# Optimization experiments

Measured on AMD Instinct MI355X. Metric: run time of the kernel, lower is better.

Reference implementation:

```python
import jax, jax.numpy as jnp
import numpy as np

D = 1024
NP = 128
BS = 2
GEO = 64
TOPK = 18

def _lin(x, w, b):
    return x @ w + b

def _mlp3(x, w1, b1, w2, b2, w3, b3):
    h = jax.nn.relu(_lin(x, w1, b1))
    h = jax.nn.relu(_lin(h, w2, b2))
    return _lin(h, w3, b3)


def setup_inputs() -> dict:
    key = jax.random.key(0)
    ks = jax.random.split(key, 24)
    feats = jax.random.normal(ks[0], (BS, NP, D), jnp.float32)
    subject = jax.random.normal(ks[1], (BS, D), jnp.float32)
    obj = jax.random.normal(ks[2], (BS, D), jnp.float32)
    # plausible boxes: xmin,ymin in [0,500), w,h in [1,101)
    xy = jax.random.uniform(ks[3], (BS, NP, 2), jnp.float32) * 500.0
    wh = jax.random.uniform(ks[4], (BS, NP, 2), jnp.float32) * 100.0 + 1.0
    prop = jnp.concatenate([xy, xy + wh], axis=-1)
    s = 0.02
    p = {}
    for i, k in zip((1, 2, 3), ks[5:8]):
        p[f"gp_w{i}"] = jax.random.normal(k, (GEO, GEO), jnp.float32) * s
        p[f"gp_b{i}"] = jnp.zeros((GEO,), jnp.float32)
    # pass_messgae: Linear(2112,1024), Linear(1024,1024), Linear(1024,1024)
    dims = [(2 * D + GEO, D), (D, D), (D, D)]
    for i, (k, (di, do)) in enumerate(zip(ks[8:11], dims), 1):
        p[f"pm_w{i}"] = jax.random.normal(k, (di, do), jnp.float32) * s
        p[f"pm_b{i}"] = jnp.zeros((do,), jnp.float32)
    # aggregate: Linear(2048,1024), Linear(1024,1024), Linear(1024,1024)
    dims = [(2 * D, D), (D, D), (D, D)]
    for i, (k, (di, do)) in enumerate(zip(ks[11:14], dims), 1):
        p[f"ag_w{i}"] = jax.random.normal(k, (di, do), jnp.float32) * s
        p[f"ag_b{i}"] = jnp.zeros((do,), jnp.float32)
    p["cs_w"] = jax.random.normal(ks[14], (2 * D, 1), jnp.float32) * s
    p["cs_b"] = jnp.zeros((1,), jnp.float32)
    p["cso_w"] = jax.random.normal(ks[15], (2 * D, 1), jnp.float32) * s
    p["cso_b"] = jnp.zeros((1,), jnp.float32)
    return dict(feats=feats, subject=subject, obj=obj, prop=prop, **p)


def _geo_embedding(prop):
    # extract_multi_position_matrix_nd with S == O == prop
    xmin, ymin, xmax, ymax = jnp.split(prop, 4, axis=-1)  # [bs,np,1]
    w = xmax - xmin + 1.0
    h = ymax - ymin + 1.0
    cx = 0.5 * (xmin + xmax)
    cy = 0.5 * (ymin + ymax)
    # [bs, np_S, np_O]
    dx = (cx - jnp.swapaxes(cx, 1, 2)) / jnp.swapaxes(w, 1, 2)
    dy = (cy - jnp.swapaxes(cy, 1, 2)) / jnp.swapaxes(h, 1, 2)
    dw = w / jnp.swapaxes(w, 1, 2)
    dh = h / jnp.swapaxes(h, 1, 2)
    pos = jnp.stack([dx, dy, dw, dh], axis=3)  # [bs,np,np,4]
    pos = jnp.log(jnp.maximum(jnp.abs(pos), 1e-3))
    # extract_pairwise_multi_position_embedding_nd, feat_dim=64, wave_length=1000
    feat_range = jnp.arange(GEO // 8, dtype=pos.dtype)
    dim_mat = jnp.power(jnp.asarray(1000.0, pos.dtype), (8.0 / GEO) * feat_range)  # [8]
    div = (100.0 * pos)[..., None] / dim_mat  # [bs,np,np,4,8]
    emb = jnp.concatenate([jnp.sin(div), jnp.cos(div)], axis=-1)  # [bs,np,np,4,16]
    return emb.reshape(*emb.shape[:3], GEO)  # [bs,np,np,64]


def reference(feats, subject, obj, prop,
              gp_w1, gp_b1, gp_w2, gp_b2, gp_w3, gp_b3,
              pm_w1, pm_b1, pm_w2, pm_b2, pm_w3, pm_b3,
              ag_w1, ag_b1, ag_w2, ag_b2, ag_w3, ag_b3,
              cs_w, cs_b, cso_w, cso_b):
    bs, num_prop, d = feats.shape
    geo = _geo_embedding(prop)                        # [bs,np,np,64]
    geo = _mlp3(geo, gp_w1, gp_b1, gp_w2, gp_b2, gp_w3, gp_b3)
    # x_1[b,i,j]=feats[b,j] ; x_2[b,i,j]=feats[b,i]  (torch unsqueeze/repeat)
    shp = (bs, num_prop, num_prop, d)
    x1 = jnp.broadcast_to(feats[:, None, :, :], shp)
    x2 = jnp.broadcast_to(feats[:, :, None, :], shp)
    pair = jnp.concatenate([x1, x2, geo], axis=-1)    # [bs,np,np,2112]
    fet = _mlp3(pair, pm_w1, pm_b1, pm_w2, pm_b2, pm_w3, pm_b3)  # [bs,np,np,1024]
    # topk over dim=2 then sum/8
    top, _ = jax.lax.top_k(jnp.swapaxes(fet, 2, 3), TOPK)  # [bs,np,1024,18]
    fet = top.sum(axis=-1) / 8.0                      # [bs,np,1024]
    x = _mlp3(jnp.concatenate([feats, fet], axis=-1),
              ag_w1, ag_b1, ag_w2, ag_b2, ag_w3, ag_b3)  # [bs,np,1024]
    sub = jnp.broadcast_to(subject[:, None, :], (bs, num_prop, d))
    ob = jnp.broadcast_to(obj[:, None, :], (bs, num_prop, d))
    x_subj = jax.nn.sigmoid(_lin(jnp.concatenate([x, sub], -1), cs_w, cs_b))[..., 0]
    x_obj = jax.nn.sigmoid(_lin(jnp.concatenate([x, ob], -1), cso_w, cso_b))[..., 0]
    return jnp.stack([x_subj, x_obj], axis=-1)        # [bs,np,2]
```

## Files before the change

kernel.cpp:

```cpp
#include <hip/hip_runtime.h>
#include <hip/hip_bf16.h>
#include <math.h>

#define D 1024
#define NP 128
#define BS 2
#define GEO 64
#define TOPKN 18
#define NPAIR (BS*NP*NP)

__device__ __forceinline__ float relu_(float x){ return fmaxf(x, 0.f); }
__device__ __forceinline__ unsigned short f2b(float x){
    __hip_bfloat16 h = __float2bfloat16(x);
    return *(unsigned short*)&h;
}
__device__ __forceinline__ float b2f(unsigned short u){
    return __uint_as_float((unsigned)u << 16);
}

typedef short bf16x8 __attribute__((ext_vector_type(8)));
typedef float f32x4  __attribute__((ext_vector_type(4)));

__device__ __forceinline__ void glds16(const unsigned short* g, unsigned short* l){
    __builtin_amdgcn_global_load_lds(
        (const __attribute__((address_space(1))) void*)g,
        (__attribute__((address_space(3))) void*)l,
        16, 0, 0);
}

#define GSTR 72
__global__ __launch_bounds__(256) void k_geo2(
    const float* __restrict__ prop,
    const float* __restrict__ gw1, const float* __restrict__ gb1,
    const float* __restrict__ gw2, const float* __restrict__ gb2,
    const float* __restrict__ gw3, const float* __restrict__ gb3,
    unsigned short* __restrict__ geoPc, int pofs)
{
    __shared__ unsigned short WT[3][GEO*GSTR];
    __shared__ float gb[3][GEO];
    __shared__ unsigned short buf[4][GEO*GSTR];
    int t = threadIdx.x, l = t & 63, w = t >> 6;

    for (int idx = t; idx < GEO*GEO; idx += 256) {
        int k = idx >> 6, n = idx & 63;
        WT[0][n*GSTR + k] = f2b(gw1[idx]);
        WT[1][n*GSTR + k] = f2b(gw2[idx]);
        WT[2][n*GSTR + k] = f2b(gw3[idx]);
    }
    if (t < GEO) { gb[0][t]=gb1[t]; gb[1][t]=gb2[t]; gb[2][t]=gb3[t]; }

    int plocal = blockIdx.x*256 + w*64;
    int pair0  = pofs + plocal;
    int c = l;
    int p = c >> 4, s = c & 15, f = s & 7;
    float dm = expf((float)f * (6.907755278982137f/8.0f));
    bool is_cos = (s & 8) != 0;
    float scale = 100.f / dm;

    int b  = pair0 >> 14;
    int ij = pair0 & 16383;
    int i  = ij >> 7;
    int j0 = ij & 127;
    float4 pi = *(const float4*)(prop + (size_t)(b*NP + i)*4);
    float wi  = pi.z-pi.x+1.f, hi_ = pi.w-pi.y+1.f;
    unsigned short* mybuf = buf[w];
    for (int r = 0; r < 64; ++r) {
        float4 pj = *(const float4*)(prop + (size_t)(b*NP + j0 + r)*4);
        float wj  = pj.z-pj.x+1.f, hj  = pj.w-pj.y+1.f;
        float pos;
        if      (p == 0) pos = (0.5f*(pi.x+pi.z) - 0.5f*(pj.x+pj.z)) / wj;
        else if (p == 1) pos = (0.5f*(pi.y+pi.w) - 0.5f*(pj.y+pj.w)) / hj;
        else if (p == 2) pos = wi / wj;
        else             pos = hi_ / hj;
        pos = logf(fmaxf(fabsf(pos), 1e-3f));
        float dv = pos * scale;
        mybuf[r*GSTR + c] = f2b(is_cos ? cosf(dv) : sinf(dv));
    }
    __syncthreads();

    int lr = l & 15, lq = l >> 4;
    #pragma unroll
    for (int layer = 0; layer < 3; ++layer) {
        const unsigned short* WTl = WT[layer];
        f32x4 acc[4][4];
        #pragma unroll
        for (int mi = 0; mi < 4; ++mi)
            #pragma unroll
            for (int ni = 0; ni < 4; ++ni)
                #pragma unroll
                for (int r = 0; r < 4; ++r) acc[mi][ni][r] = 0.f;
        #pragma unroll
        for (int kc = 0; kc < 2; ++kc) {
            bf16x8 af[4], bf[4];
            #pragma unroll
            for (int mi = 0; mi < 4; ++mi)
                af[mi] = *(const bf16x8*)(mybuf + (mi*16+lr)*GSTR + kc*32 + lq*8);
            #pragma unroll
            for (int ni = 0; ni < 4; ++ni)
                bf[ni] = *(const bf16x8*)(WTl + (ni*16+lr)*GSTR + kc*32 + lq*8);
            #pragma unroll
            for (int mi = 0; mi < 4; ++mi)
                #pragma unroll
                for (int ni = 0; ni < 4; ++ni)
                    acc[mi][ni] = __builtin_amdgcn_mfma_f32_16x16x32_bf16(af[mi], bf[ni], acc[mi][ni], 0, 0, 0);
        }
        __syncthreads();
        #pragma unroll
        for (int mi = 0; mi < 4; ++mi) {
            #pragma unroll
            for (int ni = 0; ni < 4; ++ni) {
                int col = ni*16 + lr;
                float bv = gb[layer][col];
                #pragma unroll
                for (int r = 0; r < 4; ++r) {
                    int row = mi*16 + lq*4 + r;
                    float v = acc[mi][ni][r] + bv;
                    if (layer < 2) {
                        mybuf[row*GSTR + col] = f2b(relu_(v));
                    } else {
                        geoPc[(size_t)(plocal + row)*GEO + col] = f2b(v);
                    }
                }
            }
        }
        __syncthreads();
    }
}

struct WT8 {
    const float* src[8];
    unsigned short* dst[8];
    int kt[8];
    int pre[9];
};
__global__ __launch_bounds__(256) void k_wTall(WT8 d)
{
    __shared__ float tile[64][65];
    int bid = blockIdx.x;
    int e = 0;
    while (e < 7 && bid >= d.pre[e+1]) ++e;
    int local = bid - d.pre[e];
    int bx = local & 15;
    int by = local >> 4;
    int K = d.kt[e] * 64;
    const float* W = d.src[e];
    unsigned short* WT = d.dst[e];
    int t = threadIdx.x;
    int tc = t & 63, tr = t >> 6;
    #pragma unroll
    for (int r = tr; r < 64; r += 4)
        tile[r][tc] = W[(size_t)(by*64 + r)*1024 + bx*64 + tc];
    __syncthreads();
    #pragma unroll
    for (int r = tr; r < 64; r += 4)
        WT[(size_t)(bx*64 + r)*K + by*64 + tc] = f2b(tile[tc][r]);
}

template<bool A_F32>
__global__ __launch_bounds__(256) void k_skmm(
    const void* __restrict__ A1v, const void* __restrict__ A2v,
    int K1, int K2,
    const unsigned short* __restrict__ BT0,
    const unsigned short* __restrict__ BT1,
    float* __restrict__ Cp,
    int KZ, int Kc, int N)
{
    __shared__ unsigned short As[16*32];
    __shared__ unsigned short Bs[128*32];
    int t = threadIdx.x;
    int m0 = blockIdx.x * 16;
    int n0 = blockIdx.y * 128;
    int bz = blockIdx.z;
    int kz = bz % KZ;
    int mat = bz / KZ;
    const unsigned short* BT = mat ? BT1 : BT0;
    int K = K1 + K2;
    int M = gridDim.x * 16;
    int w = t >> 6, l = t & 63;
    int lr = l & 15, lq = l >> 4;
    int arow = t >> 3, ak = (t & 7) * 4;
    int arow2 = t >> 2, ak2 = (t & 3) * 8;
    int brow = t >> 1, bk = (t & 1) * 16;
    f32x4 acc0 = {0.f,0.f,0.f,0.f}, acc1 = {0.f,0.f,0.f,0.f};
    for (int i = 0; i < Kc; i += 32) {
        int kg0 = kz*Kc + i;
        __syncthreads();
        if (A_F32) {
            if (t < 128) {
                int kg = kg0 + ak;
                const float* src = (kg < K1)
                    ? (const float*)A1v + (size_t)(m0+arow)*K1 + kg
                    : (const float*)A2v + (size_t)(m0+arow)*K2 + (kg - K1);
                float4 a4 = *(const float4*)src;
                ushort4 u;
                u.x=f2b(a4.x); u.y=f2b(a4.y); u.z=f2b(a4.z); u.w=f2b(a4.w);
                *(ushort4*)(As + arow*32 + ak) = u;
            }
        } else {
            if (t < 64) {
                const unsigned short* src = (const unsigned short*)A1v + (size_t)(m0+arow2)*K1 + kg0 + ak2;
                *(bf16x8*)(As + arow2*32 + ak2) = *(const bf16x8*)src;
            }
        }
        const unsigned short* srcb = BT + (size_t)(n0+brow)*K + kg0 + bk;
        *(bf16x8*)(Bs + brow*32 + bk)     = *(const bf16x8*)srcb;
        *(bf16x8*)(Bs + brow*32 + bk + 8) = *(const bf16x8*)(srcb + 8);
        __syncthreads();
        bf16x8 af = *(const bf16x8*)(As + lr*32 + lq*8);
        bf16x8 b0 = *(const bf16x8*)(Bs + (w*32      + lr)*32 + lq*8);
        bf16x8 b1 = *(const bf16x8*)(Bs + (w*32 + 16 + lr)*32 + lq*8);
        acc0 = __builtin_amdgcn_mfma_f32_16x16x32_bf16(af, b0, acc0, 0, 0, 0);
        acc1 = __builtin_amdgcn_mfma_f32_16x16x32_bf16(af, b1, acc1, 0, 0, 0);
    }
    float* Co = Cp + (size_t)bz*M*N;
    #pragma unroll
    for (int r = 0; r < 4; ++r) {
        int gr = m0 + lq*4 + r;
        Co[(size_t)gr*N + n0 + w*32      + lr] = acc0[r];
        Co[(size_t)gr*N + n0 + w*32 + 16 + lr] = acc1[r];
    }
}

template<bool RELU, bool OUT_BF16>
__global__ __launch_bounds__(256) void k_red(
    const float* __restrict__ Cp, int KZ,
    const float* __restrict__ bias,
    void* __restrict__ out0, void* __restrict__ out1,
    int MN, int N)
{
    int z = blockIdx.z;
    const float* C = Cp + (size_t)z*KZ*MN;
    void* out = z ? out1 : out0;
    int idx = (blockIdx.x*256 + threadIdx.x) * 4;
    f32x4 s = {0.f,0.f,0.f,0.f};
    for (int k = 0; k < KZ; ++k)
        s += *(const f32x4*)(C + (size_t)k*MN + idx);
    if (bias) s += *(const f32x4*)(bias + (idx & (N-1)));
    if (RELU) { s[0]=relu_(s[0]); s[1]=relu_(s[1]); s[2]=relu_(s[2]); s[3]=relu_(s[3]); }
    if (OUT_BF16) {
        ushort4 u; u.x=f2b(s[0]); u.y=f2b(s[1]); u.z=f2b(s[2]); u.w=f2b(s[3]);
        *(ushort4*)((unsigned short*)out + idx) = u;
    } else {
        float4 o; o.x=s[0]; o.y=s[1]; o.z=s[2]; o.w=s[3];
        *(float4*)((float*)out + idx) = o;
    }
}


#define STG(g, lb) { glds16((g) + ssrc0, (lb) + sdst0); glds16((g) + ssrc1, (lb) + sdst1); }

#define MM8_PHASE(Q, LAH, LBH, STAGE_STMT, VM)                                  \
  {                                                                             \
    if ((Q) == 0 || (Q) == 2) {                                                 \
      const char* ah = (const char*)(LAH) + ((Q) == 2 ? 16384 : 0);             \
      _Pragma("unroll")                                                         \
      for (int mi = 0; mi < 4; ++mi) {                                          \
        af[mi][0] = *(const bf16x8*)(ah + aoff[mi][0]);                         \
        af[mi][1] = *(const bf16x8*)(ah + aoff[mi][1]);                         \
      }                                                                         \
    }                                                                           \
    if ((Q) != 2) {                                                             \
      const char* bh = (const char*)(LBH) + ((Q) == 1 ? 16384 : 0);             \
      _Pragma("unroll")                                                         \
      for (int ni = 0; ni < 2; ++ni) {                                          \
        bfr[ni][0] = *(const bf16x8*)(bh + boff[ni][0]);                        \
        bfr[ni][1] = *(const bf16x8*)(bh + boff[ni][1]);                        \
      }                                                                         \
    }                                                                           \
    STAGE_STMT;                                                                 \
    asm volatile("s_waitcnt vmcnt(" #VM ")" ::: "memory");                      \
    __builtin_amdgcn_s_barrier();                                               \
    asm volatile("" ::: "memory");                                              \
    __builtin_amdgcn_s_setprio(1);                                              \
    _Pragma("unroll")                                                           \
    for (int mi = 0; mi < 4; ++mi)                                              \
      _Pragma("unroll")                                                         \
      for (int ni = 0; ni < 2; ++ni) {                                          \
        const int am = ((Q) >= 2 ? 4 : 0) + mi;                                 \
        const int an = (((Q) == 1 || (Q) == 2) ? 2 : 0) + ni;                   \
        acc[am][an] = __builtin_amdgcn_mfma_f32_16x16x32_bf16(af[mi][0], bfr[ni][0], acc[am][an], 0, 0, 0); \
        acc[am][an] = __builtin_amdgcn_mfma_f32_16x16x32_bf16(af[mi][1], bfr[ni][1], acc[am][an], 0, 0, 0); \
      }                                                                         \
    __builtin_amdgcn_s_setprio(0);                                              \
  }

template<bool RELU>
__global__ __launch_bounds__(512, 2) void k_mgemm8(
    const unsigned short* __restrict__ A,
    const unsigned short* __restrict__ BT,
    const float* __restrict__ bias,
    unsigned short* __restrict__ C, int M, int N, int K)
{
    __shared__ __align__(16) unsigned short LA[2][2][128*64];
    __shared__ __align__(16) unsigned short LB[2][2][128*64];
    int t = threadIdx.x;

    int nwg = gridDim.x * gridDim.y;
    int bid = blockIdx.y * gridDim.x + blockIdx.x;
    int wgid = (nwg & 7) ? bid : ((bid & 7) * (nwg >> 3) + (bid >> 3));
    int ntm = M >> 8;
    int tm = wgid % ntm, tn = wgid / ntm;
    int m0 = tm << 8, n0 = tn << 8;

    int w = t >> 6, l = t & 63;
    int wm = w & 1, wn = w >> 1;
    int lr = l & 15, lq = l >> 4;

    const unsigned short* Abase = A  + (size_t)m0 * K;
    const unsigned short* Bbase = BT + (size_t)n0 * K;
    int NT = K >> 6;

    size_t ssrc0, ssrc1; int sdst0, sdst1;
    {
        int o0 = t * 16;
        int s0 = o0 ^ (((o0 >> 7) & 7) << 4);
        ssrc0 = (size_t)(s0 >> 7)*K + ((s0 & 127) >> 1);
        sdst0 = o0 >> 1;
        int o1 = (512 + t) * 16;
        int s1 = o1 ^ (((o1 >> 7) & 7) << 4);
        ssrc1 = (size_t)(s1 >> 7)*K + ((s1 & 127) >> 1);
        sdst1 = o1 >> 1;
    }

    int aoff[4][2], boff[2][2];
    #pragma unroll
    for (int mi = 0; mi < 4; ++mi)
        #pragma unroll
        for (int kq = 0; kq < 2; ++kq) {
            int lo = (wm*64 + mi*16 + lr)*128 + kq*64 + lq*16;
            aoff[mi][kq] = lo ^ (((lo >> 7) & 7) << 4);
        }
    #pragma unroll
    for (int ni = 0; ni < 2; ++ni)
        #pragma unroll
        for (int kq = 0; kq < 2; ++kq) {
            int lo = (wn*32 + ni*16 + lr)*128 + kq*64 + lq*16;
            boff[ni][kq] = lo ^ (((lo >> 7) & 7) << 4);
        }

    f32x4 acc[8][4];
    #pragma unroll
    for (int i = 0; i < 8; ++i)
        #pragma unroll
        for (int j = 0; j < 4; ++j)
            #pragma unroll
            for (int r = 0; r < 4; ++r) acc[i][j][r] = 0.f;

    bf16x8 af[4][2], bfr[2][2];

    STG(Abase,                  &LA[0][0][0]);
    STG(Bbase,                  &LB[0][0][0]);
    STG(Bbase + (size_t)128*K,  &LB[0][1][0]);
    STG(Abase + (size_t)128*K,  &LA[0][1][0]);
    asm volatile("s_waitcnt vmcnt(4)" ::: "memory");
    __builtin_amdgcn_s_barrier();
    asm volatile("" ::: "memory");

    for (int kt = 0; kt < NT - 1; ++kt) {
        const unsigned short* la = &LA[kt & 1][0][0];
        const unsigned short* lb = &LB[kt & 1][0][0];
        unsigned short* nla = &LA[(kt + 1) & 1][0][0];
        unsigned short* nlb = &LB[(kt + 1) & 1][0][0];
        const unsigned short* An = Abase + (size_t)((kt + 1) << 6);
        const unsigned short* Bn = Bbase + (size_t)((kt + 1) << 6);
        MM8_PHASE(0, la, lb, STG(An, nla), 4);
        MM8_PHASE(1, la, lb, STG(Bn, nlb), 4);
        MM8_PHASE(2, la, lb, STG(Bn + (size_t)128*K, nlb + 8192), 4);
        MM8_PHASE(3, la, lb, STG(An + (size_t)128*K, nla + 8192), 4);
    }
    {
        const unsigned short* la = &LA[(NT - 1) & 1][0][0];
        const unsigned short* lb = &LB[(NT - 1) & 1][0][0];
        MM8_PHASE(0, la, lb, (void)0, 2);
        MM8_PHASE(1, la, lb, (void)0, 0);
        MM8_PHASE(2, la, lb, (void)0, 0);
        MM8_PHASE(3, la, lb, (void)0, 0);
    }

    #pragma unroll
    for (int mi = 0; mi < 8; ++mi) {
        int grow = m0 + ((mi & 4) ? 128 : 0) + wm*64 + (mi & 3)*16 + lq*4;
        #pragma unroll
        for (int ni = 0; ni < 4; ++ni) {
            int gcol = n0 + ((ni & 2) ? 128 : 0) + wn*32 + (ni & 1)*16 + lr;
            float bv = bias[gcol];
            #pragma unroll
            for (int r = 0; r < 4; ++r) {
                float v = acc[mi][ni][r] + bv;
                if (RELU) v = relu_(v);
                C[(size_t)(grow + r)*N + gcol] = f2b(v);
            }
        }
    }
}

__global__ __launch_bounds__(256) void k_h1m(
    const unsigned short* __restrict__ A,
    const unsigned short* __restrict__ BT,
    const float* __restrict__ b1,
    const unsigned short* __restrict__ U, const unsigned short* __restrict__ V,
    unsigned short* __restrict__ h1c, int pofs)
{
    __shared__ unsigned short As[2*128*32];
    __shared__ unsigned short Bs[2*128*32];
    const int K = GEO;
    int t  = threadIdx.x;
    int m0 = blockIdx.x * 128;
    int n0 = blockIdx.y * 128;
    int w  = t >> 6, l = t & 63;
    int wm = w & 1, wn = w >> 1;
    int lr = l & 15;
    int lq = l >> 4;

    int s0 = w*2, s1 = w*2 + 1;
    int srow = l >> 2;
    int sko  = (l & 3) * 8;
    int rowA0 = s0*16 + srow, rowA1 = s1*16 + srow;

    f32x4 acc[4][4];
    #pragma unroll
    for (int mi = 0; mi < 4; ++mi)
        #pragma unroll
        for (int ni = 0; ni < 4; ++ni)
            #pragma unroll
            for (int r = 0; r < 4; ++r) acc[mi][ni][r] = 0.f;

    #pragma unroll
    for (int q = 0; q < 2; ++q) {
        int kg = q*32 + sko;
        glds16(A  + (size_t)(m0 + rowA0)*K + kg, As + q*4096 + s0*512 + l*8);
        glds16(A  + (size_t)(m0 + rowA1)*K + kg, As + q*4096 + s1*512 + l*8);
        glds16(BT + (size_t)(n0 + rowA0)*K + kg, Bs + q*4096 + s0*512 + l*8);
        glds16(BT + (size_t)(n0 + rowA1)*K + kg, Bs + q*4096 + s1*512 + l*8);
    }
    __syncthreads();
    #pragma unroll
    for (int q = 0; q < 2; ++q) {
        bf16x8 af[4], bf[4];
        #pragma unroll
        for (int mi = 0; mi < 4; ++mi)
            af[mi] = *(const bf16x8*)(As + q*4096 + (wm*64 + mi*16 + lr)*32 + lq*8);
        #pragma unroll
        for (int ni = 0; ni < 4; ++ni)
            bf[ni] = *(const bf16x8*)(Bs + q*4096 + (wn*64 + ni*16 + lr)*32 + lq*8);
        #pragma unroll
        for (int mi = 0; mi < 4; ++mi)
            #pragma unroll
            for (int ni = 0; ni < 4; ++ni)
                acc[mi][ni] = __builtin_amdgcn_mfma_f32_16x16x32_bf16(af[mi], bf[ni], acc[mi][ni], 0, 0, 0);
    }

    int p0 = pofs + m0;
    int bi = p0 >> 7;
    int b  = bi >> 7;
    const unsigned short* Ubase = U + (size_t)b*NP*D;
    const unsigned short* Vrow  = V + (size_t)bi*D;
    #pragma unroll
    for (int ni = 0; ni < 4; ++ni) {
        int gc = n0 + wn*64 + ni*16 + lr;
        float add = b2f(Vrow[gc]) + b1[gc];
        #pragma unroll
        for (int mi = 0; mi < 4; ++mi) {
            int row = wm*64 + mi*16 + lq*4;
            #pragma unroll
            for (int r = 0; r < 4; ++r) {
                float u = b2f(Ubase[(size_t)(row + r)*D + gc]);
                float val = acc[mi][ni][r] + u + add;
                h1c[(size_t)(m0 + row + r)*D + gc] = f2b(relu_(val));
            }
        }
    }
}

#define TK_PAD 19
__global__ __launch_bounds__(256) void k_topk2(
    const unsigned short* __restrict__ fcb,
    float* __restrict__ red_out)
{
    __shared__ float L1[256][TK_PAD];
    __shared__ float L2[128][TK_PAD];
    int t = threadIdx.x;
    int bl = blockIdx.x;
    int cbase = blockIdx.y * 64;
    int cl = t & 63;
    int q = t >> 6;
    const unsigned short* base = fcb + (size_t)(bl*NP + q*32)*D + cbase + cl;
    float sm[TOPKN];
    #pragma unroll
    for (int x = 0; x < TOPKN; ++x) sm[x] = -INFINITY;
    for (int j = 0; j < 32; ++j) {
        float v = b2f(base[(size_t)j*D]);
        #pragma unroll
        for (int x = 0; x < TOPKN; ++x) {
            float mx = fmaxf(sm[x], v);
            v = fminf(sm[x], v);
            sm[x] = mx;
        }
    }
    #pragma unroll
    for (int x = 0; x < TOPKN; ++x) L1[t][x] = sm[x];
    __syncthreads();
    if (t < 128) {
        int h = t >> 6, cc = t & 63;
        const float* la = L1[(2*h)*64 + cc];
        const float* lb = L1[(2*h+1)*64 + cc];
        float* dst = L2[h*64 + cc];
        int ia = 0, ib = 0;
        float av = la[0], bv = lb[0];
        #pragma unroll
        for (int x = 0; x < TOPKN; ++x) {
            bool ta = (av >= bv);
            dst[x] = ta ? av : bv;
            if (ta) { ++ia; av = (ia < TOPKN) ? la[ia] : -INFINITY; }
            else    { ++ib; bv = (ib < TOPKN) ? lb[ib] : -INFINITY; }
        }
    }
    __syncthreads();
    if (t < 64) {
        const float* la = L2[t];
        const float* lb = L2[64 + t];
        int ia = 0, ib = 0;
        float av = la[0], bv = lb[0];
        float s = 0.f;
        #pragma unroll
        for (int x = 0; x < TOPKN; ++x) {
            bool ta = (av >= bv);
            s += ta ? av : bv;
            if (ta) { ++ia; av = (ia < TOPKN) ? la[ia] : -INFINITY; }
            else    { ++ib; bv = (ib < TOPKN) ? lb[ib] : -INFINITY; }
        }
        red_out[(size_t)bl*D + cbase + t] = s * 0.125f;
    }
}

__global__ __launch_bounds__(256) void k_final(const float* __restrict__ x,
    const float* __restrict__ subject, const float* __restrict__ obj,
    const float* __restrict__ cs_w, const float* __restrict__ cs_b,
    const float* __restrict__ cso_w, const float* __restrict__ cso_b,
    float* __restrict__ out)
{
    int bi = blockIdx.x;
    int b  = bi >> 7;
    const float* xr = x + (size_t)bi*D;
    const float* sb = subject + (size_t)b*D;
    const float* ob = obj + (size_t)b*D;
    int tid = threadIdx.x;
    float a0 = 0.f, a1 = 0.f;
    for (int k = tid; k < D; k += 256) {
        float xv = xr[k];
        a0 = fmaf(xv, cs_w[k], a0);
        a0 = fmaf(sb[k], cs_w[D+k], a0);
        a1 = fmaf(xv, cso_w[k], a1);
        a1 = fmaf(ob[k], cso_w[D+k], a1);
    }
    __shared__ float r0[256], r1[256];
    r0[tid] = a0; r1[tid] = a1;
    __syncthreads();
    for (int s2 = 128; s2 > 0; s2 >>= 1) {
        if (tid < s2) { r0[tid] += r0[tid+s2]; r1[tid] += r1[tid+s2]; }
        __syncthreads();
    }
    if (tid == 0) {
        out[bi*2+0] = 1.f/(1.f + expf(-(r0[0] + cs_b[0])));
        out[bi*2+1] = 1.f/(1.f + expf(-(r1[0] + cso_b[0])));
    }
}

extern "C" void kernel_launch(void* const* d_in, const int* in_sizes, int n_in,
                              void* d_out, int out_size, void* d_ws, size_t ws_size,
                              hipStream_t stream)
{
    const float* feats   = (const float*)d_in[0];
    const float* subject = (const float*)d_in[1];
    const float* obj     = (const float*)d_in[2];
    const float* prop    = (const float*)d_in[3];
    const float* gp_w1 = (const float*)d_in[4];  const float* gp_b1 = (const float*)d_in[5];
    const float* gp_w2 = (const float*)d_in[6];  const float* gp_b2 = (const float*)d_in[7];
    const float* gp_w3 = (const float*)d_in[8];  const float* gp_b3 = (const float*)d_in[9];
    const float* pm_w1 = (const float*)d_in[10]; const float* pm_b1 = (const float*)d_in[11];
    const float* pm_w2 = (const float*)d_in[12]; const float* pm_b2 = (const float*)d_in[13];
    const float* pm_w3 = (const float*)d_in[14]; const float* pm_b3 = (const float*)d_in[15];
    const float* ag_w1 = (const float*)d_in[16]; const float* ag_b1 = (const float*)d_in[17];
    const float* ag_w2 = (const float*)d_in[18]; const float* ag_b2 = (const float*)d_in[19];
    const float* ag_w3 = (const float*)d_in[20]; const float* ag_b3 = (const float*)d_in[21];
    const float* cs_w  = (const float*)d_in[22]; const float* cs_b  = (const float*)d_in[23];
    const float* cso_w = (const float*)d_in[24]; const float* cso_b = (const float*)d_in[25];
    float* out = (float*)d_out;

    const int M = BS*NP;
    const int MN = M*D;

    char* wsb = (char*)d_ws;
    size_t off = 0;
    auto alloc = [&](size_t bytes) { char* p = wsb + off; off += (bytes + 255) & ~255ull; return p; };
    unsigned short* Ub = (unsigned short*)alloc((size_t)MN*2);
    unsigned short* Vb = (unsigned short*)alloc((size_t)MN*2);
    float* red = (float*)alloc((size_t)MN*4);
    float* xf  = (float*)alloc((size_t)MN*4);
    unsigned short* xh1b = (unsigned short*)alloc((size_t)MN*2);
    unsigned short* xh2b = (unsigned short*)alloc((size_t)MN*2);
    unsigned short* w1aT = (unsigned short*)alloc((size_t)D*D*2);
    unsigned short* w1bT = (unsigned short*)alloc((size_t)D*D*2);
    unsigned short* w1cT = (unsigned short*)alloc((size_t)D*GEO*2);
    unsigned short* w2T  = (unsigned short*)alloc((size_t)D*D*2);
    unsigned short* w3T  = (unsigned short*)alloc((size_t)D*D*2);
    unsigned short* agw1T= (unsigned short*)alloc((size_t)2*D*D*2);
    unsigned short* agw2T= (unsigned short*)alloc((size_t)D*D*2);
    unsigned short* agw3T= (unsigned short*)alloc((size_t)D*D*2);
    size_t persist = off;

    size_t cp_bytes = (size_t)8*MN*4;
    size_t chunk_unit = (size_t)NP*(GEO*2 + D*2 + D*2 + D*2);
    int CH = M;
    while (CH > 2) {
        size_t region = (size_t)CH*chunk_unit;
        if (region < cp_bytes) region = cp_bytes;
        if (persist + region + 4096 <= ws_size) break;
        CH >>= 1;
    }
    float*          Cp    = (float*)(wsb + persist);
    unsigned short* geoPc = (unsigned short*)(wsb + persist);
    unsigned short* h1c   = geoPc + (size_t)CH*NP*GEO;
    unsigned short* h2c   = h1c   + (size_t)CH*NP*D;
    unsigned short* fcb   = h2c   + (size_t)CH*NP*D;

    WT8 d;
    d.src[0]=pm_w1;                d.dst[0]=w1aT;  d.kt[0]=16;
    d.src[1]=pm_w1+(size_t)D*D;    d.dst[1]=w1bT;  d.kt[1]=16;
    d.src[2]=pm_w1+(size_t)2*D*D;  d.dst[2]=w1cT;  d.kt[2]=1;
    d.src[3]=pm_w2;                d.dst[3]=w2T;   d.kt[3]=16;
    d.src[4]=pm_w3;                d.dst[4]=w3T;   d.kt[4]=16;
    d.src[5]=ag_w1;                d.dst[5]=agw1T; d.kt[5]=32;
    d.src[6]=ag_w2;                d.dst[6]=agw2T; d.kt[6]=16;
    d.src[7]=ag_w3;                d.dst[7]=agw3T; d.kt[7]=16;
    d.pre[0]=0;
    for (int e = 0; e < 8; ++e) d.pre[e+1] = d.pre[e] + d.kt[e]*16;
    k_wTall<<<d.pre[8], 256, 0, stream>>>(d);

    k_skmm<true><<<dim3(M/16, D/128, 8), 256, 0, stream>>>(
        feats, nullptr, D, 0, w1aT, w1bT, Cp, 4, 256, D);
    k_red<false,true><<<dim3(MN/1024, 1, 2), 256, 0, stream>>>(
        Cp, 4, nullptr, Ub, Vb, MN, D);

    int nchunks = M/CH;
    for (int cchunk = 0; cchunk < nchunks; ++cchunk) {
        int bi0  = cchunk * CH;
        int pofs = bi0 * NP;
        k_geo2<<<CH*NP/256, 256, 0, stream>>>(prop, gp_w1, gp_b1, gp_w2, gp_b2, gp_w3, gp_b3, geoPc, pofs);
        dim3 gBig(CH*NP/128, D/128);
        k_h1m<<<gBig, 256, 0, stream>>>(geoPc, w1cT, pm_b1, Ub, Vb, h1c, pofs);
        dim3 g8(CH*NP/256, D/256);
        k_mgemm8<true ><<<g8, 512, 0, stream>>>(h1c, w2T, pm_b2, h2c, CH*NP, D, D);
        k_mgemm8<false><<<g8, 512, 0, stream>>>(h2c, w3T, pm_b3, fcb, CH*NP, D, D);
        k_topk2<<<dim3(CH, D/64), 256, 0, stream>>>(fcb, red + (size_t)bi0*D);
    }

    k_skmm<true><<<dim3(M/16, D/128, 8), 256, 0, stream>>>(
        feats, red, D, D, agw1T, nullptr, Cp, 8, 256, D);
    k_red<true,true><<<dim3(MN/1024, 1, 1), 256, 0, stream>>>(
        Cp, 8, ag_b1, xh1b, nullptr, MN, D);
    k_skmm<false><<<dim3(M/16, D/128, 4), 256, 0, stream>>>(
        xh1b, nullptr, D, 0, agw2T, nullptr, Cp, 4, 256, D);
    k_red<true,true><<<dim3(MN/1024, 1, 1), 256, 0, stream>>>(
        Cp, 4, ag_b2, xh2b, nullptr, MN, D);
    k_skmm<false><<<dim3(M/16, D/128, 4), 256, 0, stream>>>(
        xh2b, nullptr, D, 0, agw3T, nullptr, Cp, 4, 256, D);
    k_red<false,false><<<dim3(MN/1024, 1, 1), 256, 0, stream>>>(
        Cp, 4, ag_b3, xf, nullptr, MN, D);

    k_final<<<M, 256, 0, stream>>>(xf, subject, obj, cs_w, cs_b, cso_w, cso_b, out);
}
```

Before: 461.5 us.

## Replace split-K skinny GEMMs plus reduction kernels with fused full-K GEMM epilogue

The small M=256 GEMMs (feature projections and the aggregate MLP) drop split-K partial buffers and their separate reduction kernels. Each block now loops over the full K, staging two 32-wide K slices per iteration in shared memory, and applies bias, ReLU and the bf16 conversion directly in the epilogue. This removes four reduction launches and the fp32 partial-sum traffic, and lets the chunk buffer ignore the Cp size floor. The cost is far fewer blocks (16x8 or 16x8x2), so parallelism drops and each block runs a long serial K loop.

```diff
diff --git a/kernel.cpp b/kernel.cpp
--- a/kernel.cpp
+++ b/kernel.cpp
@@ -156,93 +156,81 @@
         WT[(size_t)(bx*64 + r)*K + by*64 + tc] = f2b(tile[tc][r]);
 }
 
-template<bool A_F32>
-__global__ __launch_bounds__(256) void k_skmm(
+template<bool A_F32, bool RELU, bool OUT_BF16>
+__global__ __launch_bounds__(256) void k_skd(
     const void* __restrict__ A1v, const void* __restrict__ A2v,
     int K1, int K2,
     const unsigned short* __restrict__ BT0,
     const unsigned short* __restrict__ BT1,
-    float* __restrict__ Cp,
-    int KZ, int Kc, int N)
-{
-    __shared__ unsigned short As[16*32];
-    __shared__ unsigned short Bs[128*32];
+    const float* __restrict__ bias,
+    void* __restrict__ out0, void* __restrict__ out1, int N)
+{
+    __shared__ unsigned short As[2][16*32];
+    __shared__ unsigned short Bs[2][128*32];
     int t = threadIdx.x;
     int m0 = blockIdx.x * 16;
     int n0 = blockIdx.y * 128;
-    int bz = blockIdx.z;
-    int kz = bz % KZ;
-    int mat = bz / KZ;
+    int mat = blockIdx.z;
     const unsigned short* BT = mat ? BT1 : BT0;
+    void* outp = mat ? out1 : out0;
     int K = K1 + K2;
-    int M = gridDim.x * 16;
     int w = t >> 6, l = t & 63;
     int lr = l & 15, lq = l >> 4;
     int arow = t >> 3, ak = (t & 7) * 4;
     int arow2 = t >> 2, ak2 = (t & 3) * 8;
     int brow = t >> 1, bk = (t & 1) * 16;
     f32x4 acc0 = {0.f,0.f,0.f,0.f}, acc1 = {0.f,0.f,0.f,0.f};
-    for (int i = 0; i < Kc; i += 32) {
-        int kg0 = kz*Kc + i;
+    for (int i = 0; i < K; i += 64) {
         __syncthreads();
-        if (A_F32) {
-            if (t < 128) {
-                int kg = kg0 + ak;
-                const float* src = (kg < K1)
-                    ? (const float*)A1v + (size_t)(m0+arow)*K1 + kg
-                    : (const float*)A2v + (size_t)(m0+arow)*K2 + (kg - K1);
-                float4 a4 = *(const float4*)src;
-                ushort4 u;
-                u.x=f2b(a4.x); u.y=f2b(a4.y); u.z=f2b(a4.z); u.w=f2b(a4.w);
-                *(ushort4*)(As + arow*32 + ak) = u;
+        #pragma unroll
+        for (int h = 0; h < 2; ++h) {
+            int kg0 = i + h*32;
+            if (A_F32) {
+                if (t < 128) {
+                    int kg = kg0 + ak;
+                    const float* src = (kg < K1)
+                        ? (const float*)A1v + (size_t)(m0+arow)*K1 + kg
+                        : (const float*)A2v + (size_t)(m0+arow)*K2 + (kg - K1);
+                    float4 a4 = *(const float4*)src;
+                    ushort4 u;
+                    u.x=f2b(a4.x); u.y=f2b(a4.y); u.z=f2b(a4.z); u.w=f2b(a4.w);
+                    *(ushort4*)(As[h] + arow*32 + ak) = u;
+                }
+            } else {
+                if (t < 64) {
+                    const unsigned short* src = (const unsigned short*)A1v + (size_t)(m0+arow2)*K1 + kg0 + ak2;
+                    *(bf16x8*)(As[h] + arow2*32 + ak2) = *(const bf16x8*)src;
+                }
             }
+            const unsigned short* srcb = BT + (size_t)(n0+brow)*K + kg0 + bk;
+            *(bf16x8*)(Bs[h] + brow*32 + bk)     = *(const bf16x8*)srcb;
+            *(bf16x8*)(Bs[h] + brow*32 + bk + 8) = *(const bf16x8*)(srcb + 8);
+        }
+        __syncthreads();
+        #pragma unroll
+        for (int h = 0; h < 2; ++h) {
+            bf16x8 af = *(const bf16x8*)(As[h] + lr*32 + lq*8);
+            bf16x8 b0 = *(const bf16x8*)(Bs[h] + (w*32      + lr)*32 + lq*8);
+            bf16x8 b1 = *(const bf16x8*)(Bs[h] + (w*32 + 16 + lr)*32 + lq*8);
+            acc0 = __builtin_amdgcn_mfma_f32_16x16x32_bf16(af, b0, acc0, 0, 0, 0);
+            acc1 = __builtin_amdgcn_mfma_f32_16x16x32_bf16(af, b1, acc1, 0, 0, 0);
+        }
+    }
+    #pragma unroll
+    for (int r = 0; r < 4; ++r) {
+        int gr  = m0 + lq*4 + r;
+        int gc0 = n0 + w*32 + lr;
+        int gc1 = gc0 + 16;
+        float v0 = acc0[r] + (bias ? bias[gc0] : 0.f);
+        float v1 = acc1[r] + (bias ? bias[gc1] : 0.f);
+        if (RELU) { v0 = relu_(v0); v1 = relu_(v1); }
+        if (OUT_BF16) {
+            ((unsigned short*)outp)[(size_t)gr*N + gc0] = f2b(v0);
+            ((unsigned short*)outp)[(size_t)gr*N + gc1] = f2b(v1);
         } else {
-            if (t < 64) {
-                const unsigned short* src = (const unsigned short*)A1v + (size_t)(m0+arow2)*K1 + kg0 + ak2;
-                *(bf16x8*)(As + arow2*32 + ak2) = *(const bf16x8*)src;
-            }
-        }
-        const unsigned short* srcb = BT + (size_t)(n0+brow)*K + kg0 + bk;
-        *(bf16x8*)(Bs + brow*32 + bk)     = *(const bf16x8*)srcb;
-        *(bf16x8*)(Bs + brow*32 + bk + 8) = *(const bf16x8*)(srcb + 8);
-        __syncthreads();
-        bf16x8 af = *(const bf16x8*)(As + lr*32 + lq*8);
-        bf16x8 b0 = *(const bf16x8*)(Bs + (w*32      + lr)*32 + lq*8);
-        bf16x8 b1 = *(const bf16x8*)(Bs + (w*32 + 16 + lr)*32 + lq*8);
-        acc0 = __builtin_amdgcn_mfma_f32_16x16x32_bf16(af, b0, acc0, 0, 0, 0);
-        acc1 = __builtin_amdgcn_mfma_f32_16x16x32_bf16(af, b1, acc1, 0, 0, 0);
-    }
-    float* Co = Cp + (size_t)bz*M*N;
-    #pragma unroll
-    for (int r = 0; r < 4; ++r) {
-        int gr = m0 + lq*4 + r;
-        Co[(size_t)gr*N + n0 + w*32      + lr] = acc0[r];
-        Co[(size_t)gr*N + n0 + w*32 + 16 + lr] = acc1[r];
-    }
-}
-
-template<bool RELU, bool OUT_BF16>
-__global__ __launch_bounds__(256) void k_red(
-    const float* __restrict__ Cp, int KZ,
-    const float* __restrict__ bias,
-    void* __restrict__ out0, void* __restrict__ out1,
-    int MN, int N)
-{
-    int z = blockIdx.z;
-    const float* C = Cp + (size_t)z*KZ*MN;
-    void* out = z ? out1 : out0;
-    int idx = (blockIdx.x*256 + threadIdx.x) * 4;
-    f32x4 s = {0.f,0.f,0.f,0.f};
-    for (int k = 0; k < KZ; ++k)
-        s += *(const f32x4*)(C + (size_t)k*MN + idx);
-    if (bias) s += *(const f32x4*)(bias + (idx & (N-1)));
-    if (RELU) { s[0]=relu_(s[0]); s[1]=relu_(s[1]); s[2]=relu_(s[2]); s[3]=relu_(s[3]); }
-    if (OUT_BF16) {
-        ushort4 u; u.x=f2b(s[0]); u.y=f2b(s[1]); u.z=f2b(s[2]); u.w=f2b(s[3]);
-        *(ushort4*)((unsigned short*)out + idx) = u;
-    } else {
-        float4 o; o.x=s[0]; o.y=s[1]; o.z=s[2]; o.w=s[3];
-        *(float4*)((float*)out + idx) = o;
+            ((float*)outp)[(size_t)gr*N + gc0] = v0;
+            ((float*)outp)[(size_t)gr*N + gc1] = v1;
+        }
     }
 }
 
@@ -609,16 +597,13 @@
     unsigned short* agw3T= (unsigned short*)alloc((size_t)D*D*2);
     size_t persist = off;
 
-    size_t cp_bytes = (size_t)8*MN*4;
     size_t chunk_unit = (size_t)NP*(GEO*2 + D*2 + D*2 + D*2);
     int CH = M;
     while (CH > 2) {
         size_t region = (size_t)CH*chunk_unit;
-        if (region < cp_bytes) region = cp_bytes;
         if (persist + region + 4096 <= ws_size) break;
         CH >>= 1;
     }
-    float*          Cp    = (float*)(wsb + persist);
     unsigned short* geoPc = (unsigned short*)(wsb + persist);
     unsigned short* h1c   = geoPc + (size_t)CH*NP*GEO;
     unsigned short* h2c   = h1c   + (size_t)CH*NP*D;
@@ -637,10 +622,8 @@
     for (int e = 0; e < 8; ++e) d.pre[e+1] = d.pre[e] + d.kt[e]*16;
     k_wTall<<<d.pre[8], 256, 0, stream>>>(d);
 
-    k_skmm<true><<<dim3(M/16, D/128, 8), 256, 0, stream>>>(
-        feats, nullptr, D, 0, w1aT, w1bT, Cp, 4, 256, D);
-    k_red<false,true><<<dim3(MN/1024, 1, 2), 256, 0, stream>>>(
-        Cp, 4, nullptr, Ub, Vb, MN, D);
+    k_skd<true,false,true><<<dim3(M/16, D/128, 2), 256, 0, stream>>>(
+        feats, nullptr, D, 0, w1aT, w1bT, nullptr, Ub, Vb, D);
 
     int nchunks = M/CH;
     for (int cchunk = 0; cchunk < nchunks; ++cchunk) {
@@ -655,18 +638,12 @@
         k_topk2<<<dim3(CH, D/64), 256, 0, stream>>>(fcb, red + (size_t)bi0*D);
     }
 
-    k_skmm<true><<<dim3(M/16, D/128, 8), 256, 0, stream>>>(
-        feats, red, D, D, agw1T, nullptr, Cp, 8, 256, D);
-    k_red<true,true><<<dim3(MN/1024, 1, 1), 256, 0, stream>>>(
-        Cp, 8, ag_b1, xh1b, nullptr, MN, D);
-    k_skmm<false><<<dim3(M/16, D/128, 4), 256, 0, stream>>>(
-        xh1b, nullptr, D, 0, agw2T, nullptr, Cp, 4, 256, D);
-    k_red<true,true><<<dim3(MN/1024, 1, 1), 256, 0, stream>>>(
-        Cp, 4, ag_b2, xh2b, nullptr, MN, D);
-    k_skmm<false><<<dim3(M/16, D/128, 4), 256, 0, stream>>>(
-        xh2b, nullptr, D, 0, agw3T, nullptr, Cp, 4, 256, D);
-    k_red<false,false><<<dim3(MN/1024, 1, 1), 256, 0, stream>>>(
-        Cp, 4, ag_b3, xf, nullptr, MN, D);
+    k_skd<true,true,true><<<dim3(M/16, D/128, 1), 256, 0, stream>>>(
+        feats, red, D, D, agw1T, nullptr, ag_b1, xh1b, nullptr, D);
+    k_skd<false,true,true><<<dim3(M/16, D/128, 1), 256, 0, stream>>>(
+        xh1b, nullptr, D, 0, agw2T, nullptr, ag_b2, xh2b, nullptr, D);
+    k_skd<false,false,false><<<dim3(M/16, D/128, 1), 256, 0, stream>>>(
+        xh2b, nullptr, D, 0, agw3T, nullptr, ag_b3, xf, nullptr, D);
 
     k_final<<<M, 256, 0, stream>>>(xf, subject, obj, cs_w, cs_b, cso_w, cso_b, out);
 }
```

Measured after the change: 512.0 us. +10.9%, slower.

## Fuse top-k reduction into final pass-message GEMM epilogue

Applied to the files above, without the earlier changes.

The third pass-message GEMM no longer writes its bf16 output to global memory for a separate top-k kernel. Instead, each 256x256 tile transposes its accumulators through shared memory, and 256 threads each run an insertion top-18 over the 128 rows of one column, writing the scaled sum directly. This removes a large global write and read plus one kernel launch, and the smaller per-chunk workspace may allow bigger chunks. In exchange, shared memory grows to about 135KB, which may limit occupancy, the top-k phase runs on only half the threads, and top-k now sees fp32 values rather than bf16-rounded ones.

```diff
diff --git a/kernel.cpp b/kernel.cpp
--- a/kernel.cpp
+++ b/kernel.cpp
@@ -284,15 +284,16 @@
     __builtin_amdgcn_s_setprio(0);                                              \
   }
 
-template<bool RELU>
+template<bool RELU, bool TOPK>
 __global__ __launch_bounds__(512, 2) void k_mgemm8(
     const unsigned short* __restrict__ A,
     const unsigned short* __restrict__ BT,
     const float* __restrict__ bias,
-    unsigned short* __restrict__ C, int M, int N, int K)
-{
-    __shared__ __align__(16) unsigned short LA[2][2][128*64];
-    __shared__ __align__(16) unsigned short LB[2][2][128*64];
+    void* __restrict__ Cv, int M, int N, int K)
+{
+    __shared__ __align__(16) char SMEM[256*132*4];
+    unsigned short* LAp = (unsigned short*)SMEM;
+    unsigned short* LBp = LAp + 32768;
     int t = threadIdx.x;
 
     int nwg = gridDim.x * gridDim.y;
@@ -348,19 +349,19 @@
 
     bf16x8 af[4][2], bfr[2][2];
 
-    STG(Abase,                  &LA[0][0][0]);
-    STG(Bbase,                  &LB[0][0][0]);
-    STG(Bbase + (size_t)128*K,  &LB[0][1][0]);
-    STG(Abase + (size_t)128*K,  &LA[0][1][0]);
+    STG(Abase,                  LAp);
+    STG(Bbase,                  LBp);
+    STG(Bbase + (size_t)128*K,  LBp + 8192);
+    STG(Abase + (size_t)128*K,  LAp + 8192);
     asm volatile("s_waitcnt vmcnt(4)" ::: "memory");
     __builtin_amdgcn_s_barrier();
     asm volatile("" ::: "memory");
 
     for (int kt = 0; kt < NT - 1; ++kt) {
-        const unsigned short* la = &LA[kt & 1][0][0];
-        const unsigned short* lb = &LB[kt & 1][0][0];
-        unsigned short* nla = &LA[(kt + 1) & 1][0][0];
-        unsigned short* nlb = &LB[(kt + 1) & 1][0][0];
+        const unsigned short* la = LAp + (kt & 1)*16384;
+        const unsigned short* lb = LBp + (kt & 1)*16384;
+        unsigned short* nla = LAp + ((kt + 1) & 1)*16384;
+        unsigned short* nlb = LBp + ((kt + 1) & 1)*16384;
         const unsigned short* An = Abase + (size_t)((kt + 1) << 6);
         const unsigned short* Bn = Bbase + (size_t)((kt + 1) << 6);
         MM8_PHASE(0, la, lb, STG(An, nla), 4);
@@ -369,26 +370,71 @@
         MM8_PHASE(3, la, lb, STG(An + (size_t)128*K, nla + 8192), 4);
     }
     {
-        const unsigned short* la = &LA[(NT - 1) & 1][0][0];
-        const unsigned short* lb = &LB[(NT - 1) & 1][0][0];
+        const unsigned short* la = LAp + ((NT - 1) & 1)*16384;
+        const unsigned short* lb = LBp + ((NT - 1) & 1)*16384;
         MM8_PHASE(0, la, lb, (void)0, 2);
         MM8_PHASE(1, la, lb, (void)0, 0);
         MM8_PHASE(2, la, lb, (void)0, 0);
         MM8_PHASE(3, la, lb, (void)0, 0);
     }
 
-    #pragma unroll
-    for (int mi = 0; mi < 8; ++mi) {
-        int grow = m0 + ((mi & 4) ? 128 : 0) + wm*64 + (mi & 3)*16 + lq*4;
-        #pragma unroll
-        for (int ni = 0; ni < 4; ++ni) {
-            int gcol = n0 + ((ni & 2) ? 128 : 0) + wn*32 + (ni & 1)*16 + lr;
-            float bv = bias[gcol];
-            #pragma unroll
-            for (int r = 0; r < 4; ++r) {
-                float v = acc[mi][ni][r] + bv;
-                if (RELU) v = relu_(v);
-                C[(size_t)(grow + r)*N + gcol] = f2b(v);
+    if (!TOPK) {
+        unsigned short* C = (unsigned short*)Cv;
+        #pragma unroll
+        for (int mi = 0; mi < 8; ++mi) {
+            int grow = m0 + ((mi & 4) ? 128 : 0) + wm*64 + (mi & 3)*16 + lq*4;
+            #pragma unroll
+            for (int ni = 0; ni < 4; ++ni) {
+                int gcol = n0 + ((ni & 2) ? 128 : 0) + wn*32 + (ni & 1)*16 + lr;
+                float bv = bias[gcol];
+                #pragma unroll
+                for (int r = 0; r < 4; ++r) {
+                    float v = acc[mi][ni][r] + bv;
+                    if (RELU) v = relu_(v);
+                    C[(size_t)(grow + r)*N + gcol] = f2b(v);
+                }
+            }
+        }
+    } else {
+        float* TP = (float*)SMEM;
+        float* redp = (float*)Cv;
+        #pragma unroll
+        for (int h = 0; h < 2; ++h) {
+            __syncthreads();
+            #pragma unroll
+            for (int mi4 = 0; mi4 < 4; ++mi4) {
+                int j0 = wm*64 + mi4*16 + lq*4;
+                #pragma unroll
+                for (int ni = 0; ni < 4; ++ni) {
+                    int colLocal = ((ni & 2) ? 128 : 0) + wn*32 + (ni & 1)*16 + lr;
+                    float bv = bias[n0 + colLocal];
+                    f32x4 v;
+                    #pragma unroll
+                    for (int r = 0; r < 4; ++r) v[r] = acc[h*4 + mi4][ni][r] + bv;
+                    *(f32x4*)(TP + colLocal*132 + j0) = v;
+                }
+            }
+            __syncthreads();
+            if (t < 256) {
+                const float* col = TP + t*132;
+                float sm[TOPKN];
+                #pragma unroll
+                for (int x = 0; x < TOPKN; ++x) sm[x] = -INFINITY;
+                for (int j = 0; j < 128; ++j) {
+                    float v = col[j];
+                    if (v > sm[TOPKN-1]) {
+                        #pragma unroll
+                        for (int x = 0; x < TOPKN; ++x) {
+                            float mx = fmaxf(sm[x], v);
+                            v = fminf(sm[x], v);
+                            sm[x] = mx;
+                        }
+                    }
+                }
+                float s = 0.f;
+                #pragma unroll
+                for (int x = 0; x < TOPKN; ++x) s += sm[x];
+                redp[(size_t)((m0 >> 7) + h)*N + n0 + t] = s * 0.125f;
             }
         }
     }
@@ -469,67 +515,6 @@
                 h1c[(size_t)(m0 + row + r)*D + gc] = f2b(relu_(val));
             }
         }
-    }
-}
-
-#define TK_PAD 19
-__global__ __launch_bounds__(256) void k_topk2(
-    const unsigned short* __restrict__ fcb,
-    float* __restrict__ red_out)
-{
-    __shared__ float L1[256][TK_PAD];
-    __shared__ float L2[128][TK_PAD];
-    int t = threadIdx.x;
-    int bl = blockIdx.x;
-    int cbase = blockIdx.y * 64;
-    int cl = t & 63;
-    int q = t >> 6;
-    const unsigned short* base = fcb + (size_t)(bl*NP + q*32)*D + cbase + cl;
-    float sm[TOPKN];
-    #pragma unroll
-    for (int x = 0; x < TOPKN; ++x) sm[x] = -INFINITY;
-    for (int j = 0; j < 32; ++j) {
-        float v = b2f(base[(size_t)j*D]);
-        #pragma unroll
-        for (int x = 0; x < TOPKN; ++x) {
-            float mx = fmaxf(sm[x], v);
-            v = fminf(sm[x], v);
-            sm[x] = mx;
-        }
-    }
-    #pragma unroll
-    for (int x = 0; x < TOPKN; ++x) L1[t][x] = sm[x];
-    __syncthreads();
-    if (t < 128) {
-        int h = t >> 6, cc = t & 63;
-        const float* la = L1[(2*h)*64 + cc];
-        const float* lb = L1[(2*h+1)*64 + cc];
-        float* dst = L2[h*64 + cc];
-        int ia = 0, ib = 0;
-        float av = la[0], bv = lb[0];
-        #pragma unroll
-        for (int x = 0; x < TOPKN; ++x) {
-            bool ta = (av >= bv);
-            dst[x] = ta ? av : bv;
-            if (ta) { ++ia; av = (ia < TOPKN) ? la[ia] : -INFINITY; }
-            else    { ++ib; bv = (ib < TOPKN) ? lb[ib] : -INFINITY; }
-        }
-    }
-    __syncthreads();
-    if (t < 64) {
-        const float* la = L2[t];
-        const float* lb = L2[64 + t];
-        int ia = 0, ib = 0;
-        float av = la[0], bv = lb[0];
-        float s = 0.f;
-        #pragma unroll
-        for (int x = 0; x < TOPKN; ++x) {
-            bool ta = (av >= bv);
-            s += ta ? av : bv;
-            if (ta) { ++ia; av = (ia < TOPKN) ? la[ia] : -INFINITY; }
-            else    { ++ib; bv = (ib < TOPKN) ? lb[ib] : -INFINITY; }
-        }
-        red_out[(size_t)bl*D + cbase + t] = s * 0.125f;
     }
 }
 
@@ -610,7 +595,7 @@
     size_t persist = off;
 
     size_t cp_bytes = (size_t)8*MN*4;
-    size_t chunk_unit = (size_t)NP*(GEO*2 + D*2 + D*2 + D*2);
+    size_t chunk_unit = (size_t)NP*(GEO*2 + D*2 + D*2);
     int CH = M;
     while (CH > 2) {
         size_t region = (size_t)CH*chunk_unit;
@@ -622,7 +607,6 @@
     unsigned short* geoPc = (unsigned short*)(wsb + persist);
     unsigned short* h1c   = geoPc + (size_t)CH*NP*GEO;
     unsigned short* h2c   = h1c   + (size_t)CH*NP*D;
-    unsigned short* fcb   = h2c   + (size_t)CH*NP*D;
 
     WT8 d;
     d.src[0]=pm_w1;                d.dst[0]=w1aT;  d.kt[0]=16;
@@ -650,9 +634,8 @@
         dim3 gBig(CH*NP/128, D/128);
         k_h1m<<<gBig, 256, 0, stream>>>(geoPc, w1cT, pm_b1, Ub, Vb, h1c, pofs);
         dim3 g8(CH*NP/256, D/256);
-        k_mgemm8<true ><<<g8, 512, 0, stream>>>(h1c, w2T, pm_b2, h2c, CH*NP, D, D);
-        k_mgemm8<false><<<g8, 512, 0, stream>>>(h2c, w3T, pm_b3, fcb, CH*NP, D, D);
-        k_topk2<<<dim3(CH, D/64), 256, 0, stream>>>(fcb, red + (size_t)bi0*D);
+        k_mgemm8<true ,false><<<g8, 512, 0, stream>>>(h1c, w2T, pm_b2, h2c, CH*NP, D, D);
+        k_mgemm8<false,true ><<<g8, 512, 0, stream>>>(h2c, w3T, pm_b3, red + (size_t)bi0*D, CH*NP, D, D);
     }
 
     k_skmm<true><<<dim3(M/16, D/128, 8), 256, 0, stream>>>(
```

Result: no change. 458.1 us (-0.7%).
